# Kernel optimization log

Hardware: AMD Instinct MI355X
Metric: run time of the kernel (lower is better)

The kernel has to match this reference:

```python
import jax, jax.numpy as jnp
import numpy as np
import math

S = 30.0
M = 0.5
COS_M = math.cos(M)
SIN_M = math.sin(M)
TH = math.cos(math.pi - M)
MM = math.sin(math.pi - M) * M
B, D, C = 512, 512, 100000


def setup_inputs() -> dict:
    key = jax.random.key(0)
    k1, k2, k3 = jax.random.split(key, 3)
    inp = jax.random.normal(k1, (B, D), dtype=jnp.float32)
    weight = jax.random.normal(k2, (C, D), dtype=jnp.float32) * (1.0 / math.sqrt(D))
    label = jax.random.randint(k3, (B,), 0, C, dtype=jnp.int64)
    return {"input": inp, "label": label, "weight": weight}


def _l2norm(x, axis=-1, eps=1e-12):
    # matches F.normalize: x / max(||x||, eps)
    n = jnp.sqrt(jnp.sum(x * x, axis=axis, keepdims=True))
    return x / jnp.maximum(n, eps)


def reference(input, label, weight):
    # cosine: [B, C]
    cosine = jnp.clip(_l2norm(input) @ _l2norm(weight).T, -1.0, 1.0)
    sine = jnp.sqrt(jnp.clip(1.0 - cosine * cosine, 1e-9, 1.0))
    phi = cosine * COS_M - sine * SIN_M
    phi = jnp.where(cosine > TH, phi, cosine - MM)  # easy_margin=False branch
    one_hot = (label[:, None] == jnp.arange(cosine.shape[1])[None, :])
    out = jnp.where(one_hot, phi, cosine) * S
    return out
```

## Files before the change

kernel.cpp:

```cpp
#include <hip/hip_runtime.h>
#include <hip/hip_bf16.h>

#define ARC_S    30.0f
#define ARC_COSM 0.8775825618903728f
#define ARC_SINM 0.4794255386042030f
#define ARC_TH  -0.8775825618903728f
#define ARC_MM   0.2397127693021015f

#define B_ROWS 512
#define D_DIM  512
#define C_CLS  100000
#define C_PAD  100096

typedef float  floatx4 __attribute__((ext_vector_type(4)));
typedef __bf16 bf16x8  __attribute__((ext_vector_type(8)));

__global__ __launch_bounds__(256) void normalize_rows_512(
    const float* __restrict__ src, __bf16* __restrict__ dst, int valid_rows)
{
    const int lane = threadIdx.x & 63;
    const int wave = threadIdx.x >> 6;
    const long long row = (long long)blockIdx.x * 4 + wave;

    __bf16* drow = dst + row * D_DIM;

    if (row >= valid_rows) {
        bf16x8 z;
        #pragma unroll
        for (int i = 0; i < 8; i++) z[i] = (__bf16)0.0f;
        *(bf16x8*)(drow + lane * 8) = z;
        return;
    }

    const float4* rp = (const float4*)(src + row * D_DIM);
    float4 p0 = rp[lane * 2];
    float4 p1 = rp[lane * 2 + 1];

    float ss = p0.x*p0.x + p0.y*p0.y + p0.z*p0.z + p0.w*p0.w
             + p1.x*p1.x + p1.y*p1.y + p1.z*p1.z + p1.w*p1.w;
    #pragma unroll
    for (int m = 32; m >= 1; m >>= 1) ss += __shfl_xor(ss, m, 64);

    const float scale = 1.0f / fmaxf(sqrtf(ss), 1e-12f);

    bf16x8 v;
    v[0] = (__bf16)(p0.x * scale);
    v[1] = (__bf16)(p0.y * scale);
    v[2] = (__bf16)(p0.z * scale);
    v[3] = (__bf16)(p0.w * scale);
    v[4] = (__bf16)(p1.x * scale);
    v[5] = (__bf16)(p1.y * scale);
    v[6] = (__bf16)(p1.z * scale);
    v[7] = (__bf16)(p1.w * scale);
    *(bf16x8*)(drow + lane * 8) = v;
}

#define BM 256
#define BN 128
#define BK 32
#define KSTEPS  (D_DIM / BK)
#define N_TILES 782
#define GRID_B  1568

__device__ inline void async_load_16B(__bf16* lds, const __bf16* gmem)
{
    __builtin_amdgcn_global_load_lds(
        (const __attribute__((address_space(1))) void*)gmem,
        (__attribute__((address_space(3))) void*)lds,
        16, 0, 0);
}

__global__ __launch_bounds__(512, 4) void gemm_arcface(
    const __bf16* __restrict__ A,
    const __bf16* __restrict__ W,
    const int*    __restrict__ label,
    float*        __restrict__ out)
{
    const int b  = blockIdx.x;
    const int nt = (b & 7) + 8 * (b >> 4);
    const int mt = (b >> 3) & 1;
    if (nt >= N_TILES) return;

    __shared__ __bf16 As[2][BM * BK];
    __shared__ __bf16 Bs[2][BN * BK];
    __shared__ int    sLab[BM];

    const int tid = threadIdx.x;
    const int m0  = mt * BM;
    const int n0  = nt * BN;

    if (tid < BM) sLab[tid] = label[m0 + tid];

    const int lane = tid & 63;
    const int wave = tid >> 6;
    const int wr   = wave >> 1;
    const int wc   = wave & 1;
    const int frow = lane & 15;
    const int fch  = lane >> 4;

    const int srow = tid >> 2;
    const int skc  = (tid & 3) ^ ((tid >> 3) & 3);

    const __bf16* gA0 = A + (long long)(m0 + srow) * D_DIM + skc * 8;
    const __bf16* gA1 = gA0 + (long long)128 * D_DIM;
    const __bf16* gB0 = W + (long long)(n0 + srow) * D_DIM + skc * 8;

    int aoff[4], boff[4];
    #pragma unroll
    for (int i = 0; i < 4; i++) {
        const int ar = wr * 64 + i * 16 + frow;
        aoff[i] = ar * BK + ((fch ^ ((ar >> 1) & 3)) << 3);
        const int br = wc * 64 + i * 16 + frow;
        boff[i] = br * BK + ((fch ^ ((br >> 1) & 3)) << 3);
    }

    floatx4 acc[4][4];
    #pragma unroll
    for (int i = 0; i < 4; i++)
        #pragma unroll
        for (int j = 0; j < 4; j++)
            acc[i][j] = (floatx4)(0.0f);

    async_load_16B(&As[0][tid * 8],         gA0);
    async_load_16B(&As[0][(tid + 512) * 8], gA1);
    async_load_16B(&Bs[0][tid * 8],         gB0);
    __syncthreads();

    #pragma unroll 2
    for (int t = 0; t < KSTEPS; ++t) {
        const int cur = t & 1;
        if (t + 1 < KSTEPS) {
            const int ko = (t + 1) * BK;
            async_load_16B(&As[cur ^ 1][tid * 8],         gA0 + ko);
            async_load_16B(&As[cur ^ 1][(tid + 512) * 8], gA1 + ko);
            async_load_16B(&Bs[cur ^ 1][tid * 8],         gB0 + ko);
        }

        bf16x8 a[4], bb[4];
        #pragma unroll
        for (int i = 0; i < 4; i++) a[i]  = *(const bf16x8*)(&As[cur][aoff[i]]);
        #pragma unroll
        for (int j = 0; j < 4; j++) bb[j] = *(const bf16x8*)(&Bs[cur][boff[j]]);

        __builtin_amdgcn_s_setprio(1);
        #pragma unroll
        for (int i = 0; i < 4; i++)
            #pragma unroll
            for (int j = 0; j < 4; j++)
                acc[i][j] = __builtin_amdgcn_mfma_f32_16x16x32_bf16(
                    a[i], bb[j], acc[i][j], 0, 0, 0);
        __builtin_amdgcn_s_setprio(0);

        if (t + 1 < KSTEPS) __syncthreads();
    }

    const int mrow = (lane >> 4) * 4;
    const int ncol = lane & 15;

    #pragma unroll
    for (int i = 0; i < 4; i++) {
        #pragma unroll
        for (int r = 0; r < 4; r++) {
            const int ml  = wr * 64 + i * 16 + mrow + r;
            const int m   = m0 + ml;
            const int lab = sLab[ml];
            float* orow = out + (long long)m * C_CLS;
            #pragma unroll
            for (int j = 0; j < 4; j++) {
                const int cls = n0 + wc * 64 + j * 16 + ncol;
                if (cls < C_CLS) {
                    float c = fminf(fmaxf(acc[i][j][r], -1.0f), 1.0f);
                    float t = fminf(fmaxf(1.0f - c * c, 1e-9f), 1.0f);
                    float s = sqrtf(t);
                    float phi = c * ARC_COSM - s * ARC_SINM;
                    phi = (c > ARC_TH) ? phi : (c - ARC_MM);
                    float o = ((lab == cls) ? phi : c) * ARC_S;
                    orow[cls] = o;
                }
            }
        }
    }
}

extern "C" void kernel_launch(void* const* d_in, const int* in_sizes, int n_in,
                              void* d_out, int out_size, void* d_ws, size_t ws_size,
                              hipStream_t stream)
{
    const float* inp    = (const float*)d_in[0];
    const int*   label  = (const int*)d_in[1];
    const float* weight = (const float*)d_in[2];
    float*       out    = (float*)d_out;

    __bf16* A = (__bf16*)d_ws;
    __bf16* W = A + (size_t)B_ROWS * D_DIM;

    normalize_rows_512<<<B_ROWS / 4, 256, 0, stream>>>(inp, A, B_ROWS);
    normalize_rows_512<<<C_PAD / 4, 256, 0, stream>>>(weight, W, C_CLS);
    gemm_arcface<<<GRID_B, 512, 0, stream>>>(A, W, label, out);
}
```

Before: 443.8 us.

## Triple-buffer W tiles with explicit vmcnt waits and skip margin math off-label

The W operand moves to a three-stage LDS ring so its loads run two K-steps ahead, while A stays double-buffered. Explicit s_waitcnt vmcnt counts plus raw s_barrier replace __syncthreads, so each step waits only for the loads it needs. The loop is fully unrolled so the buffer indices are compile-time constants. The epilogue now computes sqrt/phi only for the label column instead of for every element, at the cost of extra LDS use and hand-tuned wait counts that must match the number of loads in flight.

```diff
diff --git a/kernel.cpp b/kernel.cpp
--- a/kernel.cpp
+++ b/kernel.cpp
@@ -62,6 +62,9 @@
 #define N_TILES 782
 #define GRID_B  1568
 
+#define WAITVM(N) asm volatile("s_waitcnt vmcnt(" #N ")" ::: "memory")
+#define BARRIER() asm volatile("s_barrier" ::: "memory")
+
 __device__ inline void async_load_16B(__bf16* lds, const __bf16* gmem)
 {
     __builtin_amdgcn_global_load_lds(
@@ -82,7 +85,7 @@
     if (nt >= N_TILES) return;
 
     __shared__ __bf16 As[2][BM * BK];
-    __shared__ __bf16 Bs[2][BN * BK];
+    __shared__ __bf16 Bs[3][BN * BK];
     __shared__ int    sLab[BM];
 
     const int tid = threadIdx.x;
@@ -124,23 +127,32 @@
     async_load_16B(&As[0][tid * 8],         gA0);
     async_load_16B(&As[0][(tid + 512) * 8], gA1);
     async_load_16B(&Bs[0][tid * 8],         gB0);
-    __syncthreads();
-
-    #pragma unroll 2
+    async_load_16B(&Bs[1][tid * 8],         gB0 + BK);
+
+    #pragma unroll
     for (int t = 0; t < KSTEPS; ++t) {
-        const int cur = t & 1;
         if (t + 1 < KSTEPS) {
-            const int ko = (t + 1) * BK;
-            async_load_16B(&As[cur ^ 1][tid * 8],         gA0 + ko);
-            async_load_16B(&As[cur ^ 1][(tid + 512) * 8], gA1 + ko);
-            async_load_16B(&Bs[cur ^ 1][tid * 8],         gB0 + ko);
+            const int u = t + 1;
+            async_load_16B(&As[u & 1][tid * 8],         gA0 + u * BK);
+            async_load_16B(&As[u & 1][(tid + 512) * 8], gA1 + u * BK);
         }
-
+        if (t + 2 < KSTEPS) {
+            const int u = t + 2;
+            async_load_16B(&Bs[u % 3][tid * 8],         gB0 + u * BK);
+        }
+
+        if (t <= KSTEPS - 3)      WAITVM(4);
+        else if (t == KSTEPS - 2) WAITVM(3);
+        else                      WAITVM(0);
+        BARRIER();
+
+        const __bf16* as = &As[t & 1][0];
+        const __bf16* bs = &Bs[t % 3][0];
         bf16x8 a[4], bb[4];
         #pragma unroll
-        for (int i = 0; i < 4; i++) a[i]  = *(const bf16x8*)(&As[cur][aoff[i]]);
-        #pragma unroll
-        for (int j = 0; j < 4; j++) bb[j] = *(const bf16x8*)(&Bs[cur][boff[j]]);
+        for (int i = 0; i < 4; i++) a[i]  = *(const bf16x8*)(as + aoff[i]);
+        #pragma unroll
+        for (int j = 0; j < 4; j++) bb[j] = *(const bf16x8*)(bs + boff[j]);
 
         __builtin_amdgcn_s_setprio(1);
         #pragma unroll
@@ -151,7 +163,7 @@
                     a[i], bb[j], acc[i][j], 0, 0, 0);
         __builtin_amdgcn_s_setprio(0);
 
-        if (t + 1 < KSTEPS) __syncthreads();
+        if (t + 1 < KSTEPS) BARRIER();
     }
 
     const int mrow = (lane >> 4) * 4;
@@ -170,11 +182,14 @@
                 const int cls = n0 + wc * 64 + j * 16 + ncol;
                 if (cls < C_CLS) {
                     float c = fminf(fmaxf(acc[i][j][r], -1.0f), 1.0f);
-                    float t = fminf(fmaxf(1.0f - c * c, 1e-9f), 1.0f);
-                    float s = sqrtf(t);
-                    float phi = c * ARC_COSM - s * ARC_SINM;
-                    phi = (c > ARC_TH) ? phi : (c - ARC_MM);
-                    float o = ((lab == cls) ? phi : c) * ARC_S;
+                    float o = c * ARC_S;
+                    if (lab == cls) {
+                        float tt  = fminf(fmaxf(1.0f - c * c, 1e-9f), 1.0f);
+                        float s   = sqrtf(tt);
+                        float phi = c * ARC_COSM - s * ARC_SINM;
+                        phi = (c > ARC_TH) ? phi : (c - ARC_MM);
+                        o = phi * ARC_S;
+                    }
                     orow[cls] = o;
                 }
             }
```

After: 430.4 us. 1.03x faster.
